# Kernel tuning notes

Hardware: AMD Instinct MI355X
Metric: run time of the kernel (lower is better)

The kernel has to match this reference:

```python
import jax, jax.numpy as jnp
import numpy as np

RADIUS = 2.0      # ball radius (meters)
NSAMPLE = 32      # max neighbors per ball
B = 4             # number of scenes (batch)
NPB = 4096        # points per scene (equal counts assumed)
C = 20            # number of semantic classes
CUBE = 20.0       # points live in a [0,20]^3 m cube


def setup_inputs() -> dict:
    key = jax.random.key(0)
    k1, k2, k3 = jax.random.split(key, 3)
    xyz = jax.random.uniform(k1, (B * NPB, 3), jnp.float32) * CUBE
    pred = jax.random.normal(k2, (B * NPB, C), jnp.float32)
    labels = jax.random.randint(k3, (B * NPB,), 0, C)
    tgt = jax.nn.one_hot(labels, C, dtype=jnp.float32)
    cnt = jnp.full((B,), NPB, dtype=jnp.int32)
    # module asserts new_xyz == xyz and equal batch counts
    return {"xyz": xyz, "xyz_batch_cnt": cnt, "pred": pred, "tgt": tgt,
            "new_xyz": xyz, "new_xyz_batch_cnt": cnt}


def _ball_query(xyz_b, new_xyz_b, radius, nsample):
    """xyz_b, new_xyz_b: (B, n, 3). Returns local idx (B, n, nsample).
    Replicates pointnet2 stack ball_query: first `nsample` points (in index
    order) with squared distance < radius^2; unfilled slots repeat the first
    found index. Indices are local to each batch segment."""
    n = xyz_b.shape[1]
    d2 = jnp.sum((new_xyz_b[:, :, None, :] - xyz_b[:, None, :, :]) ** 2, axis=-1)  # (B,n,n)
    mask = d2 < radius * radius
    # score = point index if inside ball else sentinel n; smallest scores = first hits
    score = jnp.where(mask, jnp.arange(n, dtype=jnp.int32), jnp.int32(n))
    neg_vals, _ = jax.lax.top_k(-score, nsample)   # largest of -score == smallest score
    idx = -neg_vals                                # (B,n,nsample), ascending index order
    first = idx[:, :, :1]                          # first found index (self is always in-ball)
    idx = jnp.where(idx == n, first, idx)          # fill empty slots with first index
    return idx


def _group(feats_b, idx_b):
    """feats_b: (B, n, C); idx_b: (B, m, nsample) local indices -> (B, m, nsample, C)."""
    b = jnp.arange(feats_b.shape[0])[:, None, None]
    return feats_b[b, idx_b]


def reference(xyz, xyz_batch_cnt, pred, tgt, new_xyz, new_xyz_batch_cnt):
    nb = xyz_batch_cnt.shape[0]
    n = xyz.shape[0] // nb                 # equal per-batch counts
    xyz_b = xyz.reshape(nb, n, 3)
    new_xyz_b = new_xyz.reshape(nb, n, 3)

    idx_b = _ball_query(xyz_b, new_xyz_b, RADIUS, NSAMPLE)   # (B,n,ns)
    m = nb * n
    idx = idx_b.reshape(m, NSAMPLE)

    # grouping_operation -> (M, C, nsample)
    grouped_pred = _group(pred.reshape(nb, n, -1), idx_b).reshape(m, NSAMPLE, -1).transpose(0, 2, 1)
    grouped_tgt = _group(tgt.reshape(nb, n, -1), idx_b).reshape(m, NSAMPLE, -1).transpose(0, 2, 1)

    # since new_xyz == xyz, every ball contains its own center -> empty_ball_mask
    # is all-False and the nonempty filtering in the torch code is the identity.
    pred_local_relation = grouped_pred - pred[:, :, None]
    tgt_local_relation = grouped_tgt - tgt[:, :, None]

    # weight (computed under no_grad in torch)
    eq = idx == idx[:, :1]
    not_eq = ~eq
    not_eq = not_eq.at[:, 0].set(True)
    a = not_eq.astype(jnp.float32)
    weight = a / jnp.sum(a, axis=-1, keepdims=True)
    return (pred_local_relation, tgt_local_relation, weight)
```

## Files before the change

kernel.cpp:

```cpp
#include <hip/hip_runtime.h>

#define NS 32
#define GD 10
#define NC3 (GD * GD * GD)
#define CAP 32
#define INV_CELL 0.5f
#define MARGIN 1e-3f

__global__ __launch_bounds__(256) void bin_kernel(
    const float* __restrict__ xyz, int n, int total,
    int* __restrict__ cnt, float4* __restrict__ cellpts)
{
    int i = blockIdx.x * 256 + threadIdx.x;
    if (i >= total) return;
    int b  = i / n;
    int il = i - b * n;
    float x = xyz[3 * i + 0], y = xyz[3 * i + 1], z = xyz[3 * i + 2];
    int cx = min(max((int)floorf(x * INV_CELL), 0), GD - 1);
    int cy = min(max((int)floorf(y * INV_CELL), 0), GD - 1);
    int cz = min(max((int)floorf(z * INV_CELL), 0), GD - 1);
    int cell = ((b * GD + cx) * GD + cy) * GD + cz;
    int pos = atomicAdd(&cnt[cell], 1);
    if (pos < CAP)
        cellpts[(size_t)cell * CAP + pos] = make_float4(x, y, z, __int_as_float(il));
}

__global__ __launch_bounds__(256) void sort_cells_kernel(
    const int* __restrict__ cnt, float4* __restrict__ cellpts, int ncells)
{
    const int half = threadIdx.x >> 5;
    const int l32  = threadIdx.x & 31;
    const int cell = blockIdx.x * 8 + half;
    if (cell >= ncells) return;
    int cc = cnt[cell];
    cc = cc < CAP ? cc : CAP;
    if (cc <= 1) return;

    float4 f = make_float4(0.f, 0.f, 0.f, 0.f);
    int key = 0x7fffffff;
    if (l32 < cc) {
        f   = cellpts[(size_t)cell * CAP + l32];
        key = __float_as_int(f.w);
    }
    int src = l32;

    #pragma unroll
    for (int k = 2; k <= 32; k <<= 1) {
        #pragma unroll
        for (int j = k >> 1; j >= 1; j >>= 1) {
            const int  ok    = __shfl_xor(key, j, 32);
            const int  os    = __shfl_xor(src, j, 32);
            const bool up    = ((l32 & k) == 0);
            const bool lower = ((l32 & j) == 0);
            const bool takeMin = (lower == up);
            const bool keep = takeMin ? (key <= ok) : (key >= ok);
            key = keep ? key : ok;
            src = keep ? src : os;
        }
    }
    const float sx = __shfl(f.x, src, 32);
    const float sy = __shfl(f.y, src, 32);
    const float sz = __shfl(f.z, src, 32);
    const float sw = __shfl(f.w, src, 32);
    if (l32 < cc)
        cellpts[(size_t)cell * CAP + l32] = make_float4(sx, sy, sz, sw);
}

template <int C>
__global__ __launch_bounds__(256) void query_kernel(
    const float* __restrict__ new_xyz,
    const float* __restrict__ pred, const float* __restrict__ tgt,
    const int* __restrict__ cnt, const float4* __restrict__ cellpts,
    int n, int total,
    float* __restrict__ out0, float* __restrict__ out1, float* __restrict__ wout)
{
#pragma clang fp contract(off)
    __shared__ int spref[4][65];
    __shared__ int sgb[4][64];
    __shared__ int slist[4][64];

    const int lane = threadIdx.x & 63;
    const int wv   = __builtin_amdgcn_readfirstlane(threadIdx.x >> 6);
    int q = blockIdx.x * 4 + wv;
    if (q >= total) q = total - 1;
    const int b    = q / n;
    const int base = b * n;

    const float qx = new_xyz[q * 3 + 0];
    const float qy = new_xyz[q * 3 + 1];
    const float qz = new_xyz[q * 3 + 2];

    int cx0 = max((int)floorf((qx - 2.0f - MARGIN) * INV_CELL), 0);
    int cx1 = min((int)floorf((qx + 2.0f + MARGIN) * INV_CELL), GD - 1);
    int cy0 = max((int)floorf((qy - 2.0f - MARGIN) * INV_CELL), 0);
    int cy1 = min((int)floorf((qy + 2.0f + MARGIN) * INV_CELL), GD - 1);
    int cz0 = max((int)floorf((qz - 2.0f - MARGIN) * INV_CELL), 0);
    int cz1 = min((int)floorf((qz + 2.0f + MARGIN) * INV_CELL), GD - 1);
    const int ny = cy1 - cy0 + 1, nz = cz1 - cz0 + 1;
    const int ncell = __builtin_amdgcn_readfirstlane((cx1 - cx0 + 1) * ny * nz);

    int cc = 0, gbase = 0;
    if (lane < ncell) {
        int lx  = lane / (ny * nz);
        int rem = lane - lx * (ny * nz);
        int ly  = rem / nz;
        int lz  = rem - ly * nz;
        int cell = ((b * GD + (cx0 + lx)) * GD + (cy0 + ly)) * GD + (cz0 + lz);
        int c = cnt[cell];
        cc    = c < CAP ? c : CAP;
        gbase = cell * CAP;
    }
    int run = cc;
    #pragma unroll
    for (int off = 1; off < 64; off <<= 1) {
        int y = __shfl_up(run, off, 64);
        if (lane >= off) run += y;
    }
    const int T = __shfl(run, ncell - 1, 64);

    spref[wv][lane + 1] = run;
    if (lane == 0) spref[wv][0] = 0;
    if (lane < ncell) sgb[wv][lane] = gbase;

    __syncthreads();

    int tot = 0;
    for (int r = 0; r < T; r += 64) {
        const int  t   = r + lane;
        const bool act = t < T;
        const int  tcl = act ? t : 0;
        int k = 0;
        #pragma unroll
        for (int step = 32; step >= 1; step >>= 1) {
            const int nk = k + step;
            if (spref[wv][nk] <= tcl) k = nk;
        }
        const int ai = sgb[wv][k] + (tcl - spref[wv][k]);
        const float4 f = cellpts[ai];
        float dx = qx - f.x, dy = qy - f.y, dz = qz - f.z;
        float d2 = (dx * dx + dy * dy) + dz * dz;
        const bool hit = act && (d2 < 4.0f);
        const unsigned long long m = __ballot(hit);
        const int pos = tot + __builtin_amdgcn_mbcnt_hi(
            (unsigned)(m >> 32), __builtin_amdgcn_mbcnt_lo((unsigned)m, 0u));
        if (hit && pos < 64) slist[wv][pos] = __float_as_int(f.w);
        tot += __popcll(m);
    }

    __syncthreads();

    const int totv = tot < 64 ? tot : 64;
    int v = (lane < totv) ? slist[wv][lane] : 0x7fffffff;
    #pragma unroll
    for (int k = 2; k <= 64; k <<= 1) {
        #pragma unroll
        for (int j = k >> 1; j >= 1; j >>= 1) {
            const int  o     = __shfl_xor(v, j, 64);
            const bool up    = ((lane & k) == 0);
            const bool lower = ((lane & j) == 0);
            const int  mn = v < o ? v : o;
            const int  mx = v < o ? o : v;
            v = (lower == up) ? mn : mx;
        }
    }

    const int tc     = tot < NS ? tot : NS;
    const int firstv = __shfl(v, 0, 64);
    const int first  = (tot > 0) ? firstv : (n - 1);
    const int s      = lane & 31;
    const int jl0    = __shfl(v, s, 64);
    const int jl     = (s < tc) ? jl0 : first;

    const int tcm = tc > 0 ? tc : 1;
    if (lane < NS)
        wout[(size_t)q * NS + lane] = (lane < tcm) ? 1.0f / (float)tcm : 0.0f;

    const float* __restrict__ src = (lane >> 5) ? tgt : pred;
    float* __restrict__ dst       = (lane >> 5) ? out1 : out0;
    const float4* __restrict__ nb = (const float4*)(src + (size_t)(base + jl) * C);
    const float4* __restrict__ ct = (const float4*)(src + (size_t)q * C);
    float* __restrict__ o = dst + (size_t)q * (C * NS) + s;
    #pragma unroll
    for (int c4 = 0; c4 < C / 4; ++c4) {
        const float4 a = nb[c4], bq = ct[c4];
        o[(c4 * 4 + 0) * NS] = a.x - bq.x;
        o[(c4 * 4 + 1) * NS] = a.y - bq.y;
        o[(c4 * 4 + 2) * NS] = a.z - bq.z;
        o[(c4 * 4 + 3) * NS] = a.w - bq.w;
    }
    #pragma unroll
    for (int c = (C / 4) * 4; c < C; ++c)
        o[c * NS] = src[(size_t)(base + jl) * C + c] - src[(size_t)q * C + c];
}

template <int C>
__global__ __launch_bounds__(256) void fused_brute_kernel(
    const float* __restrict__ xyz, const float* __restrict__ new_xyz,
    const float* __restrict__ pred, const float* __restrict__ tgt,
    int n, int total, float* __restrict__ out0, float* __restrict__ out1,
    float* __restrict__ wout)
{
#pragma clang fp contract(off)
    __shared__ int sidx[8][NS];

    const int lane = threadIdx.x & 63;
    const int wv   = __builtin_amdgcn_readfirstlane(threadIdx.x >> 6);
    int q0 = (blockIdx.x * 4 + wv) * 2;
    if (q0 > total - 2) q0 = total - 2;
    const int base = (q0 / n) * n;

    const float ax0 = new_xyz[q0 * 3 + 0], ay0 = new_xyz[q0 * 3 + 1], az0 = new_xyz[q0 * 3 + 2];
    const float ax1 = new_xyz[q0 * 3 + 3], ay1 = new_xyz[q0 * 3 + 4], az1 = new_xyz[q0 * 3 + 5];
    const float* __restrict__ px = xyz + (size_t)base * 3;

    int tot0 = 0, tot1 = 0, first0 = n - 1, first1 = n - 1;
    for (int it = 0; it < n; it += 64) {
        const int ja  = it + lane;
        const int jca = ja < n ? ja : n - 1;
        const float xa = px[jca * 3 + 0], ya = px[jca * 3 + 1], za = px[jca * 3 + 2];
        float dx = ax0 - xa, dy = ay0 - ya, dz = az0 - za;
        const float d0 = (dx * dx + dy * dy) + dz * dz;
        dx = ax1 - xa; dy = ay1 - ya; dz = az1 - za;
        const float d1 = (dx * dx + dy * dy) + dz * dz;
        const bool h0 = (ja < n) & (d0 < 4.0f);
        const bool h1 = (ja < n) & (d1 < 4.0f);
        const unsigned long long m0 = __ballot(h0);
        if (m0) {
            if (tot0 == 0) first0 = it + __builtin_ctzll(m0);
            const int pos = tot0 + __builtin_amdgcn_mbcnt_hi(
                (unsigned)(m0 >> 32), __builtin_amdgcn_mbcnt_lo((unsigned)m0, 0u));
            if (h0 && pos < NS) sidx[wv * 2 + 0][pos] = ja;
            tot0 += __popcll(m0);
        }
        const unsigned long long m1 = __ballot(h1);
        if (m1) {
            if (tot1 == 0) first1 = it + __builtin_ctzll(m1);
            const int pos = tot1 + __builtin_amdgcn_mbcnt_hi(
                (unsigned)(m1 >> 32), __builtin_amdgcn_mbcnt_lo((unsigned)m1, 0u));
            if (h1 && pos < NS) sidx[wv * 2 + 1][pos] = ja;
            tot1 += __popcll(m1);
        }
    }

    const int s  = lane & 31;
    const int qs = lane >> 5;
    {
        const int tt    = qs ? tot1 : tot0;
        const int first = qs ? first1 : first0;
        const int tc    = tt < NS ? tt : NS;
        if (s >= tc) sidx[wv * 2 + qs][s] = first;
        const int tcm = tc > 0 ? tc : 1;
        wout[(size_t)q0 * NS + lane] = (s < tcm) ? 1.0f / (float)tcm : 0.0f;
    }
    __syncthreads();

    const int q  = q0 + qs;
    const int jl = sidx[wv * 2 + qs][s];
    const float4* __restrict__ nb_p = (const float4*)(pred + (size_t)(base + jl) * C);
    const float4* __restrict__ nb_t = (const float4*)(tgt  + (size_t)(base + jl) * C);
    const float4* __restrict__ ct_p = (const float4*)(pred + (size_t)q * C);
    const float4* __restrict__ ct_t = (const float4*)(tgt  + (size_t)q * C);
    float* __restrict__ o0 = out0 + (size_t)q * (C * NS) + s;
    float* __restrict__ o1 = out1 + (size_t)q * (C * NS) + s;
    #pragma unroll
    for (int c4 = 0; c4 < C / 4; ++c4) {
        const float4 a = nb_p[c4], bq = ct_p[c4];
        o0[(c4 * 4 + 0) * NS] = a.x - bq.x;
        o0[(c4 * 4 + 1) * NS] = a.y - bq.y;
        o0[(c4 * 4 + 2) * NS] = a.z - bq.z;
        o0[(c4 * 4 + 3) * NS] = a.w - bq.w;
        const float4 u = nb_t[c4], vv = ct_t[c4];
        o1[(c4 * 4 + 0) * NS] = u.x - vv.x;
        o1[(c4 * 4 + 1) * NS] = u.y - vv.y;
        o1[(c4 * 4 + 2) * NS] = u.z - vv.z;
        o1[(c4 * 4 + 3) * NS] = u.w - vv.w;
    }
}

extern "C" void kernel_launch(void* const* d_in, const int* in_sizes, int n_in,
                              void* d_out, int out_size, void* d_ws, size_t ws_size,
                              hipStream_t stream)
{
    const float* xyz     = (const float*)d_in[0];
    const float* pred    = (const float*)d_in[2];
    const float* tgt     = (const float*)d_in[3];
    const float* new_xyz = (const float*)d_in[4];

    const int total = in_sizes[0] / 3;
    const int nb    = in_sizes[1];
    const int n     = total / nb;
    const int C     = in_sizes[2] / total;

    float* out = (float*)d_out;
    const size_t relsz = (size_t)total * C * NS;
    float* out0 = out;
    float* out1 = out + relsz;
    float* wout = out + 2 * relsz;

    const int ncells = nb * NC3;
    const size_t ws_need = (size_t)ncells * CAP * sizeof(float4) + (size_t)ncells * sizeof(int);

    if (C == 20 && ws_size >= ws_need) {
        float4* cellpts = (float4*)d_ws;
        int*    cnt     = (int*)((char*)d_ws + (size_t)ncells * CAP * sizeof(float4));

        hipMemsetAsync(cnt, 0, (size_t)ncells * sizeof(int), stream);
        bin_kernel<<<(total + 255) / 256, 256, 0, stream>>>(xyz, n, total, cnt, cellpts);
        sort_cells_kernel<<<(ncells + 7) / 8, 256, 0, stream>>>(cnt, cellpts, ncells);
        query_kernel<20><<<(total + 3) / 4, 256, 0, stream>>>(
            new_xyz, pred, tgt, cnt, cellpts, n, total, out0, out1, wout);
    } else if (C == 20) {
        fused_brute_kernel<20><<<(total + 7) / 8, 256, 0, stream>>>(
            xyz, new_xyz, pred, tgt, n, total, out0, out1, wout);
    }
    (void)n_in; (void)out_size;
}
```

Measured before the change: 39.95 us.

## Replace fixed-capacity cell bins with per-scene counting sort and contiguous z-ranges

The memset, the global-atomic binning kernel and the per-cell bitonic sort kernel are replaced by one kernel per scene. Each block bins the scene's points in LDS using a counting sort, insertion-sorts each cell by index and writes compact point arrays with a cellStart prefix table. The query then scans contiguous z-column ranges (at most 9 instead of 27 cells) with a shorter binary search, and uses a 32-wide bitonic sort when there are few hits. This removes two launches and the CAP truncation, but only 4 blocks do the binning, which serialises that phase and uses a large LDS footprint.

```diff
diff --git a/kernel.cpp b/kernel.cpp
--- a/kernel.cpp
+++ b/kernel.cpp
@@ -3,80 +3,112 @@
 #define NS 32
 #define GD 10
 #define NC3 (GD * GD * GD)
-#define CAP 32
+#define NPB 4096
 #define INV_CELL 0.5f
 #define MARGIN 1e-3f
 
-__global__ __launch_bounds__(256) void bin_kernel(
-    const float* __restrict__ xyz, int n, int total,
-    int* __restrict__ cnt, float4* __restrict__ cellpts)
+__global__ __launch_bounds__(256) void bin_sort_kernel(
+    const float* __restrict__ xyz, int n, int nb,
+    int* __restrict__ cellStart, float4* __restrict__ pts)
 {
-    int i = blockIdx.x * 256 + threadIdx.x;
-    if (i >= total) return;
-    int b  = i / n;
-    int il = i - b * n;
-    float x = xyz[3 * i + 0], y = xyz[3 * i + 1], z = xyz[3 * i + 2];
-    int cx = min(max((int)floorf(x * INV_CELL), 0), GD - 1);
-    int cy = min(max((int)floorf(y * INV_CELL), 0), GD - 1);
-    int cz = min(max((int)floorf(z * INV_CELL), 0), GD - 1);
-    int cell = ((b * GD + cx) * GD + cy) * GD + cz;
-    int pos = atomicAdd(&cnt[cell], 1);
-    if (pos < CAP)
-        cellpts[(size_t)cell * CAP + pos] = make_float4(x, y, z, __int_as_float(il));
-}
-
-__global__ __launch_bounds__(256) void sort_cells_kernel(
-    const int* __restrict__ cnt, float4* __restrict__ cellpts, int ncells)
-{
-    const int half = threadIdx.x >> 5;
-    const int l32  = threadIdx.x & 31;
-    const int cell = blockIdx.x * 8 + half;
-    if (cell >= ncells) return;
-    int cc = cnt[cell];
-    cc = cc < CAP ? cc : CAP;
-    if (cc <= 1) return;
-
-    float4 f = make_float4(0.f, 0.f, 0.f, 0.f);
-    int key = 0x7fffffff;
-    if (l32 < cc) {
-        f   = cellpts[(size_t)cell * CAP + l32];
-        key = __float_as_int(f.w);
-    }
-    int src = l32;
-
-    #pragma unroll
-    for (int k = 2; k <= 32; k <<= 1) {
-        #pragma unroll
-        for (int j = k >> 1; j >= 1; j >>= 1) {
-            const int  ok    = __shfl_xor(key, j, 32);
-            const int  os    = __shfl_xor(src, j, 32);
-            const bool up    = ((l32 & k) == 0);
-            const bool lower = ((l32 & j) == 0);
-            const bool takeMin = (lower == up);
-            const bool keep = takeMin ? (key <= ok) : (key >= ok);
-            key = keep ? key : ok;
-            src = keep ? src : os;
-        }
-    }
-    const float sx = __shfl(f.x, src, 32);
-    const float sy = __shfl(f.y, src, 32);
-    const float sz = __shfl(f.z, src, 32);
-    const float sw = __shfl(f.w, src, 32);
-    if (l32 < cc)
-        cellpts[(size_t)cell * CAP + l32] = make_float4(sx, sy, sz, sw);
+    __shared__ int    lcnt[NC3];
+    __shared__ int    lpref[NC3];
+    __shared__ int    lcur[NC3];
+    __shared__ float4 lpts[NPB];
+    __shared__ int    wsum[4];
+
+    const int tid = threadIdx.x;
+    const int b   = blockIdx.x;
+    const float* __restrict__ px = xyz + (size_t)b * n * 3;
+
+    for (int c = tid; c < NC3; c += 256) lcnt[c] = 0;
+    __syncthreads();
+
+    for (int i = tid; i < n; i += 256) {
+        float x = px[3 * i], y = px[3 * i + 1], z = px[3 * i + 2];
+        int cx = min(max((int)floorf(x * INV_CELL), 0), GD - 1);
+        int cy = min(max((int)floorf(y * INV_CELL), 0), GD - 1);
+        int cz = min(max((int)floorf(z * INV_CELL), 0), GD - 1);
+        atomicAdd(&lcnt[(cx * GD + cy) * GD + cz], 1);
+    }
+    __syncthreads();
+
+    const int base = tid * 4;
+    int c0 = 0, c1 = 0, c2 = 0, c3 = 0, tt = 0;
+    if (base < NC3) {
+        c0 = lcnt[base];
+        c1 = base + 1 < NC3 ? lcnt[base + 1] : 0;
+        c2 = base + 2 < NC3 ? lcnt[base + 2] : 0;
+        c3 = base + 3 < NC3 ? lcnt[base + 3] : 0;
+        tt = c0 + c1 + c2 + c3;
+    }
+    const int lane = tid & 63, wv = tid >> 6;
+    int run = tt;
+    #pragma unroll
+    for (int off = 1; off < 64; off <<= 1) {
+        int y = __shfl_up(run, off, 64);
+        if (lane >= off) run += y;
+    }
+    if (lane == 63) wsum[wv] = run;
+    __syncthreads();
+    int woff = 0;
+    for (int w = 0; w < wv; ++w) woff += wsum[w];
+    const int excl = woff + run - tt;
+    if (base < NC3) {
+        lpref[base] = excl;
+        if (base + 1 < NC3) lpref[base + 1] = excl + c0;
+        if (base + 2 < NC3) lpref[base + 2] = excl + c0 + c1;
+        if (base + 3 < NC3) lpref[base + 3] = excl + c0 + c1 + c2;
+    }
+    __syncthreads();
+    for (int c = tid; c < NC3; c += 256) lcur[c] = lpref[c];
+    __syncthreads();
+
+    for (int i = tid; i < n; i += 256) {
+        float x = px[3 * i], y = px[3 * i + 1], z = px[3 * i + 2];
+        int cx = min(max((int)floorf(x * INV_CELL), 0), GD - 1);
+        int cy = min(max((int)floorf(y * INV_CELL), 0), GD - 1);
+        int cz = min(max((int)floorf(z * INV_CELL), 0), GD - 1);
+        int pos = atomicAdd(&lcur[(cx * GD + cy) * GD + cz], 1);
+        lpts[pos] = make_float4(x, y, z, __int_as_float(i));
+    }
+    __syncthreads();
+
+    #pragma unroll
+    for (int k = 0; k < 4; ++k) {
+        const int c = base + k;
+        if (c >= NC3) break;
+        const int s = lpref[c];
+        const int e = (c + 1 < NC3) ? lpref[c + 1] : n;
+        for (int i = s + 1; i < e; ++i) {
+            float4 key = lpts[i];
+            int kk = __float_as_int(key.w);
+            int j = i - 1;
+            while (j >= s && __float_as_int(lpts[j].w) > kk) {
+                lpts[j + 1] = lpts[j];
+                --j;
+            }
+            lpts[j + 1] = key;
+        }
+    }
+    __syncthreads();
+
+    for (int i = tid; i < n; i += 256) pts[(size_t)b * n + i] = lpts[i];
+    for (int c = tid; c < NC3; c += 256) cellStart[b * NC3 + c] = b * n + lpref[c];
+    if (b == nb - 1 && tid == 0) cellStart[nb * NC3] = nb * n;
 }
 
 template <int C>
 __global__ __launch_bounds__(256) void query_kernel(
     const float* __restrict__ new_xyz,
     const float* __restrict__ pred, const float* __restrict__ tgt,
-    const int* __restrict__ cnt, const float4* __restrict__ cellpts,
+    const int* __restrict__ cellStart, const float4* __restrict__ pts,
     int n, int total,
     float* __restrict__ out0, float* __restrict__ out1, float* __restrict__ wout)
 {
 #pragma clang fp contract(off)
-    __shared__ int spref[4][65];
-    __shared__ int sgb[4][64];
+    __shared__ int spref[4][17];
+    __shared__ int sgb[4][16];
     __shared__ int slist[4][64];
 
     const int lane = threadIdx.x & 63;
@@ -96,19 +128,18 @@
     int cy1 = min((int)floorf((qy + 2.0f + MARGIN) * INV_CELL), GD - 1);
     int cz0 = max((int)floorf((qz - 2.0f - MARGIN) * INV_CELL), 0);
     int cz1 = min((int)floorf((qz + 2.0f + MARGIN) * INV_CELL), GD - 1);
-    const int ny = cy1 - cy0 + 1, nz = cz1 - cz0 + 1;
-    const int ncell = __builtin_amdgcn_readfirstlane((cx1 - cx0 + 1) * ny * nz);
-
-    int cc = 0, gbase = 0;
-    if (lane < ncell) {
-        int lx  = lane / (ny * nz);
-        int rem = lane - lx * (ny * nz);
-        int ly  = rem / nz;
-        int lz  = rem - ly * nz;
-        int cell = ((b * GD + (cx0 + lx)) * GD + (cy0 + ly)) * GD + (cz0 + lz);
-        int c = cnt[cell];
-        cc    = c < CAP ? c : CAP;
-        gbase = cell * CAP;
+    const int ny = cy1 - cy0 + 1;
+    const int nrange = __builtin_amdgcn_readfirstlane((cx1 - cx0 + 1) * ny);
+
+    int cc = 0, gb = 0;
+    if (lane < nrange) {
+        int rx  = lane / ny;
+        int ry  = lane - rx * ny;
+        int col = ((b * GD + (cx0 + rx)) * GD + (cy0 + ry)) * GD;
+        int s0  = cellStart[col + cz0];
+        int s1  = cellStart[col + cz1 + 1];
+        gb = s0;
+        cc = s1 - s0;
     }
     int run = cc;
     #pragma unroll
@@ -116,11 +147,11 @@
         int y = __shfl_up(run, off, 64);
         if (lane >= off) run += y;
     }
-    const int T = __shfl(run, ncell - 1, 64);
-
-    spref[wv][lane + 1] = run;
+    const int T = __shfl(run, nrange - 1, 64);
+
+    if (lane < 16) spref[wv][lane + 1] = run;
     if (lane == 0) spref[wv][0] = 0;
-    if (lane < ncell) sgb[wv][lane] = gbase;
+    if (lane < nrange) sgb[wv][lane] = gb;
 
     __syncthreads();
 
@@ -131,12 +162,12 @@
         const int  tcl = act ? t : 0;
         int k = 0;
         #pragma unroll
-        for (int step = 32; step >= 1; step >>= 1) {
+        for (int step = 8; step >= 1; step >>= 1) {
             const int nk = k + step;
             if (spref[wv][nk] <= tcl) k = nk;
         }
         const int ai = sgb[wv][k] + (tcl - spref[wv][k]);
-        const float4 f = cellpts[ai];
+        const float4 f = pts[ai];
         float dx = qx - f.x, dy = qy - f.y, dz = qz - f.z;
         float d2 = (dx * dx + dy * dy) + dz * dz;
         const bool hit = act && (d2 < 4.0f);
@@ -151,16 +182,32 @@
 
     const int totv = tot < 64 ? tot : 64;
     int v = (lane < totv) ? slist[wv][lane] : 0x7fffffff;
-    #pragma unroll
-    for (int k = 2; k <= 64; k <<= 1) {
+    const int l32 = lane & 31;
+    if (totv <= 32) {
         #pragma unroll
-        for (int j = k >> 1; j >= 1; j >>= 1) {
-            const int  o     = __shfl_xor(v, j, 64);
-            const bool up    = ((lane & k) == 0);
-            const bool lower = ((lane & j) == 0);
-            const int  mn = v < o ? v : o;
-            const int  mx = v < o ? o : v;
-            v = (lower == up) ? mn : mx;
+        for (int k = 2; k <= 32; k <<= 1) {
+            #pragma unroll
+            for (int j = k >> 1; j >= 1; j >>= 1) {
+                const int  o     = __shfl_xor(v, j, 32);
+                const bool up    = ((l32 & k) == 0);
+                const bool lower = ((l32 & j) == 0);
+                const int  mn = v < o ? v : o;
+                const int  mx = v < o ? o : v;
+                v = (lower == up) ? mn : mx;
+            }
+        }
+    } else {
+        #pragma unroll
+        for (int k = 2; k <= 64; k <<= 1) {
+            #pragma unroll
+            for (int j = k >> 1; j >= 1; j >>= 1) {
+                const int  o     = __shfl_xor(v, j, 64);
+                const bool up    = ((lane & k) == 0);
+                const bool lower = ((lane & j) == 0);
+                const int  mn = v < o ? v : o;
+                const int  mx = v < o ? o : v;
+                v = (lower == up) ? mn : mx;
+            }
         }
     }
 
@@ -297,18 +344,16 @@
     float* out1 = out + relsz;
     float* wout = out + 2 * relsz;
 
-    const int ncells = nb * NC3;
-    const size_t ws_need = (size_t)ncells * CAP * sizeof(float4) + (size_t)ncells * sizeof(int);
-
-    if (C == 20 && ws_size >= ws_need) {
-        float4* cellpts = (float4*)d_ws;
-        int*    cnt     = (int*)((char*)d_ws + (size_t)ncells * CAP * sizeof(float4));
-
-        hipMemsetAsync(cnt, 0, (size_t)ncells * sizeof(int), stream);
-        bin_kernel<<<(total + 255) / 256, 256, 0, stream>>>(xyz, n, total, cnt, cellpts);
-        sort_cells_kernel<<<(ncells + 7) / 8, 256, 0, stream>>>(cnt, cellpts, ncells);
+    const size_t ws_need = (size_t)total * sizeof(float4)
+                         + ((size_t)nb * NC3 + 1) * sizeof(int);
+
+    if (C == 20 && n == NPB && ws_size >= ws_need) {
+        float4* pts       = (float4*)d_ws;
+        int*    cellStart = (int*)((char*)d_ws + (size_t)total * sizeof(float4));
+
+        bin_sort_kernel<<<nb, 256, 0, stream>>>(xyz, n, nb, cellStart, pts);
         query_kernel<20><<<(total + 3) / 4, 256, 0, stream>>>(
-            new_xyz, pred, tgt, cnt, cellpts, n, total, out0, out1, wout);
+            new_xyz, pred, tgt, cellStart, pts, n, total, out0, out1, wout);
     } else if (C == 20) {
         fused_brute_kernel<20><<<(total + 7) / 8, 256, 0, stream>>>(
             xyz, new_xyz, pred, tgt, n, total, out0, out1, wout);
```

Measured after the change: 51.62 us. 29.2% more time.
